# Optimization experiments

Hardware: AMD Instinct MI355X
Metric: run time of the kernel (lower is better)

Reference implementation:

```python
import jax, jax.numpy as jnp
import numpy as np
import math

N_HEAD = 16
N_EMBD = 1024
HEAD_DIM = N_EMBD // N_HEAD
B, T = 2, 2048


def setup_inputs() -> dict:
    key = jax.random.key(0)
    k1, k2, k3 = jax.random.split(key, 3)
    scale = 0.02
    x = jax.random.normal(k1, (B, T, N_EMBD), dtype=jnp.float32)
    W_attn = jax.random.normal(k2, (N_EMBD, 3 * N_EMBD), dtype=jnp.float32) * scale
    b_attn = jnp.zeros((3 * N_EMBD,), dtype=jnp.float32)
    W_proj = jax.random.normal(k3, (N_EMBD, N_EMBD), dtype=jnp.float32) * scale
    b_proj = jnp.zeros((N_EMBD,), dtype=jnp.float32)
    return {"x": x, "W_attn": W_attn, "b_attn": b_attn, "W_proj": W_proj, "b_proj": b_proj}


def reference(x, W_attn, b_attn, W_proj, b_proj):
    b, t, c = x.shape
    qkv = x @ W_attn + b_attn                      # [B,T,3C]
    q, k, v = jnp.split(qkv, 3, axis=-1)
    # [B,T,C] -> [B,H,T,D]
    def heads(z):
        return z.reshape(b, t, N_HEAD, HEAD_DIM).transpose(0, 2, 1, 3)
    q, k, v = heads(q), heads(k), heads(v)
    att = jnp.einsum('bhqd,bhkd->bhqk', q, k) * (1.0 / math.sqrt(HEAD_DIM))
    causal = jnp.tril(jnp.ones((t, t), dtype=bool))  # [T,T]
    att = jnp.where(causal[None, None], att, -jnp.inf)
    att = jax.nn.softmax(att, axis=-1)
    y = jnp.einsum('bhqk,bhkd->bhqd', att, v)      # [B,H,T,D]
    y = y.transpose(0, 2, 1, 3).reshape(b, t, c)   # [B,T,C]
    return y @ W_proj + b_proj
```

## Files before the change

kernel.cpp:

```cpp
#include <hip/hip_runtime.h>
#include <hip/hip_bf16.h>


typedef __bf16 bf16_t;
typedef __bf16 bf16x8 __attribute__((ext_vector_type(8)));
typedef float f32x4 __attribute__((ext_vector_type(4)));
typedef unsigned short ushort_t;

#define QSCALE 0.18033688011f

__device__ __forceinline__ void glds16(const bf16_t* g, ushort_t* l) {
  __builtin_amdgcn_global_load_lds(
      (const __attribute__((address_space(1))) unsigned int*)g,
      (__attribute__((address_space(3))) unsigned int*)l, 16, 0, 0);
}

__global__ __launch_bounds__(256) void prep_kernel(
    const float* __restrict__ x, const float* __restrict__ W_attn,
    const float* __restrict__ W_proj, ushort_t* __restrict__ Xb,
    ushort_t* __restrict__ WtA, ushort_t* __restrict__ WtP) {
  const int bid = blockIdx.x, tid = threadIdx.x;
  if (bid < 4096) {
    int i = bid * 256 + tid;
    float4 v = ((const float4*)x)[i];
    ushort4 o;
    o.x = __builtin_bit_cast(unsigned short, (bf16_t)v.x);
    o.y = __builtin_bit_cast(unsigned short, (bf16_t)v.y);
    o.z = __builtin_bit_cast(unsigned short, (bf16_t)v.z);
    o.w = __builtin_bit_cast(unsigned short, (bf16_t)v.w);
    ((ushort4*)Xb)[i] = o;
    return;
  }
  __shared__ ushort_t tile[32][33];
  const float* in;
  ushort_t* out;
  int C, bx, by;
  if (bid < 4096 + 3072) { int idx = bid - 4096; in = W_attn; out = WtA; C = 3072; bx = idx % 96; by = idx / 96; }
  else                   { int idx = bid - 7168; in = W_proj; out = WtP; C = 1024; bx = idx % 32; by = idx / 32; }
  const int tx = tid & 31, ty = tid >> 5;
  int cbase = bx * 32, rbase = by * 32;
#pragma unroll
  for (int i = ty; i < 32; i += 8)
    tile[i][tx] = __builtin_bit_cast(
        unsigned short, (bf16_t)in[(size_t)(rbase + i) * C + cbase + tx]);
  __syncthreads();
#pragma unroll
  for (int i = ty; i < 32; i += 8)
    out[(size_t)(cbase + i) * 1024 + rbase + tx] = tile[tx][i];
}

__global__ __launch_bounds__(512) void qkv_gemm_kernel(
    const bf16_t* __restrict__ X, const bf16_t* __restrict__ WtA,
    const float* __restrict__ bias, bf16_t* __restrict__ Qd,
    bf16_t* __restrict__ Kd, bf16_t* __restrict__ Vtd) {
  __shared__ ushort_t As[2 * 2 * 256 * 32];
  __shared__ ushort_t Bs[2 * 2 * 192 * 32];
  const int tid  = threadIdx.x;
  const int lane = tid & 63, wave = tid >> 6;
  const int l15  = lane & 15, quad = lane >> 4;
  const int wrow = (wave >> 1) * 64;
  const int wcol = (wave & 1) * 96;
  const int mtile = blockIdx.x * 256, ntile = blockIdx.y * 192;
  const int K = 1024;
  const int lr4 = lane >> 2;
  const int csw = ((lane & 3) ^ ((lr4 >> 1) & 3)) * 8;
  const int rsw = (quad ^ ((l15 >> 1) & 3)) * 8;
  const bf16_t* Xrow = X   + (size_t)(mtile + lr4) * K + csw;
  const bf16_t* Wrow = WtA + (size_t)(ntile + lr4) * K + csw;

#define STAGE_QKV(kb, Asl, Bsl)                                              \
  {                                                                          \
    _Pragma("unroll")                                                        \
    for (int kk = 0; kk < 7; kk++) {                                         \
      int s = wave + kk * 8;                                                 \
      if (s < 32) {                                                          \
        int hh = s >> 4, r16 = s & 15;                                       \
        glds16(Xrow + (size_t)(r16 * 16) * K + (kb) + hh * 32,               \
               (Asl) + hh * 8192 + r16 * 512);                               \
      } else {                                                               \
        int sb = s - 32;                                                     \
        int hh = (sb >= 12) ? 1 : 0, r12 = sb - hh * 12;                     \
        glds16(Wrow + (size_t)(r12 * 16) * K + (kb) + hh * 32,               \
               (Bsl) + hh * 6144 + r12 * 512);                               \
      }                                                                      \
    }                                                                        \
  }

  f32x4 acc[4][6] = {};
  STAGE_QKV(0, As, Bs);
  __syncthreads();
  for (int kt = 0; kt < 16; kt++) {
    const int cur = kt & 1, nxt = cur ^ 1;
    if (kt + 1 < 16)
      STAGE_QKV((kt + 1) * 64, As + nxt * 16384, Bs + nxt * 12288);
#pragma unroll
    for (int hh = 0; hh < 2; hh++) {
      bf16x8 af[4], bfr[6];
#pragma unroll
      for (int i = 0; i < 4; i++)
        af[i] = *(const bf16x8*)&As[cur * 16384 + hh * 8192 + (wrow + i * 16 + l15) * 32 + rsw];
#pragma unroll
      for (int j = 0; j < 6; j++)
        bfr[j] = *(const bf16x8*)&Bs[cur * 12288 + hh * 6144 + (wcol + j * 16 + l15) * 32 + rsw];
#pragma unroll
      for (int i = 0; i < 4; i++)
#pragma unroll
        for (int j = 0; j < 6; j++)
          acc[i][j] = __builtin_amdgcn_mfma_f32_16x16x32_bf16(af[i], bfr[j], acc[i][j], 0, 0, 0);
    }
    __syncthreads();
  }
#undef STAGE_QKV

  const int b = mtile >> 11;
#pragma unroll
  for (int j = 0; j < 6; j++) {
    int n = ntile + wcol + j * 16 + l15;
    float bv = bias[n];
    int sec = n >> 10, cc = n & 1023, h = cc >> 6, d = cc & 63;
    size_t bh = (size_t)(b * 16 + h);
    if (sec == 2) {
#pragma unroll
      for (int i = 0; i < 4; i++) {
        int tbase = (mtile & 2047) + wrow + i * 16 + quad * 4;
        ushort4 o4;
        o4.x = __builtin_bit_cast(unsigned short, (bf16_t)(acc[i][j][0] + bv));
        o4.y = __builtin_bit_cast(unsigned short, (bf16_t)(acc[i][j][1] + bv));
        o4.z = __builtin_bit_cast(unsigned short, (bf16_t)(acc[i][j][2] + bv));
        o4.w = __builtin_bit_cast(unsigned short, (bf16_t)(acc[i][j][3] + bv));
        *(ushort4*)&Vtd[(bh * 64 + d) * 2048 + tbase] = o4;
      }
    } else {
      const float sv = (sec == 0) ? QSCALE : 1.0f;
      bf16_t* Od = (sec == 0) ? Qd : Kd;
#pragma unroll
      for (int i = 0; i < 4; i++) {
#pragma unroll
        for (int r = 0; r < 4; r++) {
          int t = (mtile & 2047) + wrow + i * 16 + quad * 4 + r;
          Od[(bh * 2048 + t) * 64 + d] = (bf16_t)((acc[i][j][r] + bv) * sv);
        }
      }
    }
  }
}

__global__ __launch_bounds__(512) void attn_kernel(
    const bf16_t* __restrict__ Q, const bf16_t* __restrict__ K,
    const bf16_t* __restrict__ Vt, bf16_t* __restrict__ Y) {
  __shared__ ushort_t Ks[2][4096];
  __shared__ ushort_t Vs[2][4096];
  __shared__ ushort_t Ps[8][16 * 40];
  const int bh = blockIdx.y;
  const int qt = (blockIdx.y < 16) ? (15 - (int)blockIdx.x) : (int)blockIdx.x;
  const int tid = threadIdx.x, wave = tid >> 6, lane = tid & 63;
  const int l15 = lane & 15, quad = lane >> 4;
  const bf16_t* Qh = Q + (size_t)bh * 2048 * 64;
  const bf16_t* Kh = K + (size_t)bh * 2048 * 64;
  const bf16_t* Vh = Vt + (size_t)bh * 64 * 2048;
  const int b = bh >> 4, h = bh & 15;
  const int qw = qt * 128 + wave * 16;
  const int nkt = 2 * qt + 2;

  bf16x8 qa[2];
#pragma unroll
  for (int kc = 0; kc < 2; kc++)
    qa[kc] = *(const bf16x8*)(Qh + (size_t)(qw + l15) * 64 + kc * 32 + quad * 8);

  f32x4 o[4] = {};
  float lpart[4] = {};
  const int rsw = (quad ^ ((l15 >> 1) & 3)) * 8;

  const int lr4 = lane >> 2;
  const int csw = ((lane & 3) ^ ((lr4 >> 1) & 3)) * 8;
  const bool isK = wave < 4;
  const int sw = isK ? wave : wave - 4;
  const int rbase = (sw & 1) * 32;
  const bf16_t* gp0;
  size_t rowstep;
  if (isK) { gp0 = Kh + (size_t)(rbase + lr4) * 64 + (sw >> 1) * 32 + csw;  rowstep = 64; }
  else     { gp0 = Vh + (size_t)(rbase + lr4) * 2048 + (sw >> 1) * 32 + csw; rowstep = 2048; }
  const size_t kstep = isK ? (size_t)64 * 64 : 64;
  ushort_t* dst0 = (isK ? Ks[0] : Vs[0]) + (sw >> 1) * 2048 + rbase * 32;
  ushort_t* dst1 = (isK ? Ks[1] : Vs[1]) + (sw >> 1) * 2048 + rbase * 32;

#pragma unroll
  for (int c = 0; c < 2; c++)
    glds16(gp0 + (size_t)(c * 16) * rowstep, dst0 + c * 512);

  f32x4 zz = {0.f, 0.f, 0.f, 0.f};
  for (int kt = 0; kt < nkt; kt++) {
    const int cur = kt & 1;
    __syncthreads();
    if (kt + 1 < nkt) {
      ushort_t* nd = cur ? dst0 : dst1;
#pragma unroll
      for (int c = 0; c < 2; c++)
        glds16(gp0 + (size_t)(kt + 1) * kstep + (size_t)(c * 16) * rowstep, nd + c * 512);
    }
#pragma unroll
    for (int h32 = 0; h32 < 2; h32++) {
      const int kb32 = kt * 64 + h32 * 32;
      if (kb32 > qw + 15) break;
      bf16x8 kb[2][2];
#pragma unroll
      for (int bn = 0; bn < 2; bn++)
#pragma unroll
        for (int kc = 0; kc < 2; kc++)
          kb[bn][kc] = *(const bf16x8*)&Ks[cur][kc * 2048 + (h32 * 32 + bn * 16 + l15) * 32 + rsw];
      f32x4 s[2];
#pragma unroll
      for (int bn = 0; bn < 2; bn++) {
        f32x4 t0 = __builtin_amdgcn_mfma_f32_16x16x32_bf16(qa[0], kb[bn][0], zz, 0, 0, 0);
        s[bn] = __builtin_amdgcn_mfma_f32_16x16x32_bf16(qa[1], kb[bn][1], t0, 0, 0, 0);
      }
      const bool dg = (kb32 + 31 > qw);
#pragma unroll
      for (int r = 0; r < 4; r++) {
        int row = qw + quad * 4 + r;
        float v0 = s[0][r];
        float v1 = s[1][r];
        if (dg) {
          int c0 = kb32 + l15;
          if (c0 > row) v0 = -1e5f;
          if (c0 + 16 > row) v1 = -1e5f;
        }
        float p0 = __builtin_amdgcn_exp2f(v0);
        float p1 = __builtin_amdgcn_exp2f(v1);
        lpart[r] += p0 + p1;
        int prow = (quad * 4 + r) * 40;
        Ps[wave][prow + l15]      = __builtin_bit_cast(unsigned short, (bf16_t)p0);
        Ps[wave][prow + 16 + l15] = __builtin_bit_cast(unsigned short, (bf16_t)p1);
      }
      bf16x8 vb[4];
#pragma unroll
      for (int ns = 0; ns < 4; ns++)
        vb[ns] = *(const bf16x8*)&Vs[cur][h32 * 2048 + (ns * 16 + l15) * 32 + rsw];
      __asm__ volatile("" ::: "memory");
      bf16x8 pa = *(const bf16x8*)&Ps[wave][l15 * 40 + quad * 8];
#pragma unroll
      for (int ns = 0; ns < 4; ns++)
        o[ns] = __builtin_amdgcn_mfma_f32_16x16x32_bf16(pa, vb[ns], o[ns], 0, 0, 0);
    }
  }
#pragma unroll
  for (int r = 0; r < 4; r++) {
    float l = lpart[r];
#pragma unroll
    for (int off = 1; off < 16; off <<= 1) l += __shfl_xor(l, off);
    float inv_l = 1.0f / fmaxf(l, 1e-30f);
    int t = qw + quad * 4 + r;
#pragma unroll
    for (int ns = 0; ns < 4; ns++) {
      int c = h * 64 + ns * 16 + l15;
      Y[((size_t)(b * 2048 + t)) * 1024 + c] = (bf16_t)(o[ns][r] * inv_l);
    }
  }
}

__global__ __launch_bounds__(256) void proj_gemm_kernel(
    const bf16_t* __restrict__ Yb, const bf16_t* __restrict__ WtP,
    const float* __restrict__ bias, float* __restrict__ out) {
  __shared__ ushort_t As[128 * 32];
  __shared__ ushort_t Bs[64 * 32];
  const int tid = threadIdx.x;
  const int lane = tid & 63, wave = tid >> 6;
  const int l15 = lane & 15, quad = lane >> 4;
  const int wrow = (wave >> 1) * 64, wcol = (wave & 1) * 32;
  const int mtile = blockIdx.x * 128, ntile = blockIdx.y * 64;
  const int K = 1024;
  const int lr = lane >> 2;
  const int lc = (((lane & 3) ^ ((lr >> 1) & 3)) * 8);
  const bf16_t* Ap = Yb + (size_t)(mtile + wave * 32 + lr) * K + lc;
  const bf16_t* Bp = WtP + (size_t)(ntile + wave * 16 + lr) * K + lc;
  const int rsw = (quad ^ ((l15 >> 1) & 3)) * 8;
  ushort_t* Asw = As + wave * 32 * 32;
  ushort_t* Bsw = Bs + wave * 16 * 32;
  f32x4 acc[4][2] = {};
  for (int kb = 0; kb < K; kb += 32) {
    __syncthreads();
    glds16(Ap + kb, Asw);
    glds16(Ap + (size_t)16 * K + kb, Asw + 16 * 32);
    glds16(Bp + kb, Bsw);
    __syncthreads();
    bf16x8 af[4], bfr[2];
#pragma unroll
    for (int i = 0; i < 4; i++)
      af[i] = *(const bf16x8*)&As[(wrow + i * 16 + l15) * 32 + rsw];
#pragma unroll
    for (int j = 0; j < 2; j++)
      bfr[j] = *(const bf16x8*)&Bs[(wcol + j * 16 + l15) * 32 + rsw];
#pragma unroll
    for (int i = 0; i < 4; i++)
#pragma unroll
      for (int j = 0; j < 2; j++)
        acc[i][j] = __builtin_amdgcn_mfma_f32_16x16x32_bf16(af[i], bfr[j], acc[i][j], 0, 0, 0);
  }
#pragma unroll
  for (int j = 0; j < 2; j++) {
    int n = ntile + wcol + j * 16 + l15;
    float bv = bias[n];
#pragma unroll
    for (int i = 0; i < 4; i++) {
#pragma unroll
      for (int r = 0; r < 4; r++) {
        int m = mtile + wrow + i * 16 + quad * 4 + r;
        out[(size_t)m * 1024 + n] = acc[i][j][r] + bv;
      }
    }
  }
}

extern "C" void kernel_launch(void* const* d_in, const int* in_sizes, int n_in,
                              void* d_out, int out_size, void* d_ws, size_t ws_size,
                              hipStream_t stream) {
  const float* x      = (const float*)d_in[0];
  const float* W_attn = (const float*)d_in[1];
  const float* b_attn = (const float*)d_in[2];
  const float* W_proj = (const float*)d_in[3];
  const float* b_proj = (const float*)d_in[4];
  float* out = (float*)d_out;

  bf16_t* ws  = (bf16_t*)d_ws;
  bf16_t* WtA = ws;
  bf16_t* WtP = WtA + (size_t)3072 * 1024;
  bf16_t* Xb  = WtP + (size_t)1024 * 1024;
  bf16_t* Qb  = Xb + (size_t)4194304;
  bf16_t* Kb  = Qb + (size_t)4194304;
  bf16_t* Vtb = Kb + (size_t)4194304;
  bf16_t* Yb  = Vtb + (size_t)4194304;

  prep_kernel<<<8192, 256, 0, stream>>>(x, W_attn, W_proj,
      (ushort_t*)Xb, (ushort_t*)WtA, (ushort_t*)WtP);
  qkv_gemm_kernel<<<dim3(16, 16), 512, 0, stream>>>(Xb, WtA, b_attn, Qb, Kb, Vtb);
  attn_kernel<<<dim3(16, 32), 512, 0, stream>>>(Qb, Kb, Vtb, Yb);
  proj_gemm_kernel<<<dim3(32, 16), 256, 0, stream>>>(Yb, WtP, b_proj, out);
}
```

Measured before the change: 176.9 us.

## Compute transposed scores to keep P in registers, drop LDS round-trip

Swaps the MFMA operand order so the score tile comes out transposed (key rows across quads, query along lanes). Each lane's exp values then form the A operand of the PV MFMA directly, which removes the per-wave Ps shared-memory buffer and its stores and reloads. V fragments are now gathered as two 4-element LDS reads that match the reordered k index. The row-sum reduction shrinks to two cross-quad shuffles plus a broadcast at the end. The cost is more, smaller LDS reads for V and reliance on the k-permutation being consistent between P and V.

```diff
diff --git a/kernel.cpp b/kernel.cpp
--- a/kernel.cpp
+++ b/kernel.cpp
@@ -4,6 +4,7 @@
 
 typedef __bf16 bf16_t;
 typedef __bf16 bf16x8 __attribute__((ext_vector_type(8)));
+typedef __bf16 bf16x4 __attribute__((ext_vector_type(4)));
 typedef float f32x4 __attribute__((ext_vector_type(4)));
 typedef unsigned short ushort_t;
 
@@ -150,7 +151,6 @@
     const bf16_t* __restrict__ Vt, bf16_t* __restrict__ Y) {
   __shared__ ushort_t Ks[2][4096];
   __shared__ ushort_t Vs[2][4096];
-  __shared__ ushort_t Ps[8][16 * 40];
   const int bh = blockIdx.y;
   const int qt = (blockIdx.y < 16) ? (15 - (int)blockIdx.x) : (int)blockIdx.x;
   const int tid = threadIdx.x, wave = tid >> 6, lane = tid & 63;
@@ -168,8 +168,11 @@
     qa[kc] = *(const bf16x8*)(Qh + (size_t)(qw + l15) * 64 + kc * 32 + quad * 8);
 
   f32x4 o[4] = {};
-  float lpart[4] = {};
+  float lp = 0.f;
   const int rsw = (quad ^ ((l15 >> 1) & 3)) * 8;
+  const int sw4 = (l15 >> 1) & 3;
+  const int vlo_off = (((quad >> 1) ^ sw4) * 8) + (quad & 1) * 4;
+  const int vhi_off = ((((quad >> 1) + 2) ^ sw4) * 8) + (quad & 1) * 4;
 
   const int lr4 = lane >> 2;
   const int csw = ((lane & 3) ^ ((lr4 >> 1) & 3)) * 8;
@@ -211,49 +214,48 @@
       f32x4 s[2];
 #pragma unroll
       for (int bn = 0; bn < 2; bn++) {
-        f32x4 t0 = __builtin_amdgcn_mfma_f32_16x16x32_bf16(qa[0], kb[bn][0], zz, 0, 0, 0);
-        s[bn] = __builtin_amdgcn_mfma_f32_16x16x32_bf16(qa[1], kb[bn][1], t0, 0, 0, 0);
+        f32x4 t0 = __builtin_amdgcn_mfma_f32_16x16x32_bf16(kb[bn][0], qa[0], zz, 0, 0, 0);
+        s[bn] = __builtin_amdgcn_mfma_f32_16x16x32_bf16(kb[bn][1], qa[1], t0, 0, 0, 0);
       }
       const bool dg = (kb32 + 31 > qw);
+      const int qrow = qw + l15;
+      bf16x8 pa;
 #pragma unroll
       for (int r = 0; r < 4; r++) {
-        int row = qw + quad * 4 + r;
         float v0 = s[0][r];
         float v1 = s[1][r];
         if (dg) {
-          int c0 = kb32 + l15;
-          if (c0 > row) v0 = -1e5f;
-          if (c0 + 16 > row) v1 = -1e5f;
+          int k0 = kb32 + quad * 4 + r;
+          if (k0 > qrow) v0 = -1e5f;
+          if (k0 + 16 > qrow) v1 = -1e5f;
         }
         float p0 = __builtin_amdgcn_exp2f(v0);
         float p1 = __builtin_amdgcn_exp2f(v1);
-        lpart[r] += p0 + p1;
-        int prow = (quad * 4 + r) * 40;
-        Ps[wave][prow + l15]      = __builtin_bit_cast(unsigned short, (bf16_t)p0);
-        Ps[wave][prow + 16 + l15] = __builtin_bit_cast(unsigned short, (bf16_t)p1);
-      }
-      bf16x8 vb[4];
-#pragma unroll
-      for (int ns = 0; ns < 4; ns++)
-        vb[ns] = *(const bf16x8*)&Vs[cur][h32 * 2048 + (ns * 16 + l15) * 32 + rsw];
-      __asm__ volatile("" ::: "memory");
-      bf16x8 pa = *(const bf16x8*)&Ps[wave][l15 * 40 + quad * 8];
-#pragma unroll
-      for (int ns = 0; ns < 4; ns++)
-        o[ns] = __builtin_amdgcn_mfma_f32_16x16x32_bf16(pa, vb[ns], o[ns], 0, 0, 0);
-    }
-  }
+        lp += p0 + p1;
+        pa[r]     = (bf16_t)p0;
+        pa[4 + r] = (bf16_t)p1;
+      }
+#pragma unroll
+      for (int ns = 0; ns < 4; ns++) {
+        const int rowoff = h32 * 2048 + (ns * 16 + l15) * 32;
+        bf16x4 vlo = *(const bf16x4*)&Vs[cur][rowoff + vlo_off];
+        bf16x4 vhi = *(const bf16x4*)&Vs[cur][rowoff + vhi_off];
+        bf16x8 vb = __builtin_shufflevector(vlo, vhi, 0, 1, 2, 3, 4, 5, 6, 7);
+        o[ns] = __builtin_amdgcn_mfma_f32_16x16x32_bf16(pa, vb, o[ns], 0, 0, 0);
+      }
+    }
+  }
+  lp += __shfl_xor(lp, 16);
+  lp += __shfl_xor(lp, 32);
+  float inv_l = 1.0f / fmaxf(lp, 1e-30f);
 #pragma unroll
   for (int r = 0; r < 4; r++) {
-    float l = lpart[r];
-#pragma unroll
-    for (int off = 1; off < 16; off <<= 1) l += __shfl_xor(l, off);
-    float inv_l = 1.0f / fmaxf(l, 1e-30f);
+    float il = __shfl(inv_l, quad * 4 + r);
     int t = qw + quad * 4 + r;
 #pragma unroll
     for (int ns = 0; ns < 4; ns++) {
       int c = h * 64 + ns * 16 + l15;
-      Y[((size_t)(b * 2048 + t)) * 1024 + c] = (bf16_t)(o[ns][r] * inv_l);
+      Y[((size_t)(b * 2048 + t)) * 1024 + c] = (bf16_t)(o[ns][r] * il);
     }
   }
 }
```

New measurement: 178.7 us. Within noise of the previous version (+1.0%).
